# Optimization experiments

Measured on AMD Instinct MI355X. Metric: run time of the kernel, lower is better.

## Reference

```python
import jax, jax.numpy as jnp
import numpy as np

EMBED_DIM = 128
N_EMBED = 10000
INPUT_SHAPE = (8, 64, 32, EMBED_DIM)


def setup_inputs() -> dict:
    key = jax.random.key(0)
    k1, k2 = jax.random.split(key)
    inputs = jax.random.normal(k1, INPUT_SHAPE, dtype=jnp.float32)
    cluster_mean = jax.random.normal(k2, (EMBED_DIM, N_EMBED), dtype=jnp.float32)
    return {"inputs": inputs, "cluster_mean": cluster_mean}


def reference(inputs, cluster_mean):
    embed_dim = cluster_mean.shape[0]
    # Flatten all leading dims: (N, D)
    samples = inputs.reshape(-1, embed_dim)
    # Squared euclidean distance to each code: (N, n_embed)
    dist = (
        jnp.sum(samples ** 2, axis=1, keepdims=True)
        - 2.0 * samples @ cluster_mean
        + jnp.sum(cluster_mean ** 2, axis=0, keepdims=True)
    )
    cluster_index = jnp.argmin(dist, axis=1).reshape(inputs.shape[:-1])
    # Embedding lookup from transposed codebook: (..., D)
    quantize = cluster_mean.T[cluster_index]
    q_loss = jnp.mean((quantize - jax.lax.stop_gradient(inputs)) ** 2)
    e_loss = jnp.mean((jax.lax.stop_gradient(quantize) - inputs) ** 2)
    loss = q_loss + 0.25 * e_loss
    # Straight-through estimator
    outputs = inputs + jax.lax.stop_gradient(quantize - inputs)
    return outputs, loss
```

## Files before the change

kernel.cpp:

```cpp
#include <hip/hip_runtime.h>

#define EMBED 128
#define NCODE 10000
#define NSAMP 16384
#define NCODE_PAD 10240
#define NSPLIT 8
#define SPLIT_CODES 1280
#define NCHUNK 20
#define CHUNK_ELEMS 8192
#define OUT_ELEMS (NSAMP * EMBED)
#define TAU 0.002f
#define NSEG 16

typedef float f32x16 __attribute__((ext_vector_type(16)));
typedef short s16x8 __attribute__((ext_vector_type(8)));
typedef unsigned short ushort_t;
typedef unsigned long long u64;

#define OFF_AH  0
#define OFF_AL  2621440
#define OFF_CT  5242880
#define OFF_CN  10485760
#define OFF_KEY 10526720
#define OFF_C2  11575296
#define OFF_IDX 12099584
#define OFF_RL  12165120
#define OFF_CNT 12230656
#define OFF_BEST 12230720

__device__ __forceinline__ unsigned short f2bf(float f) {
    unsigned u = __float_as_uint(f);
    return (unsigned short)((u + 0x7fffu + ((u >> 16) & 1u)) >> 16);
}
__device__ __forceinline__ float bf2f(unsigned short h) {
    return __uint_as_float(((unsigned)h) << 16);
}
__device__ __forceinline__ unsigned ordf(float f) {
    unsigned u = __float_as_uint(f);
    return (u & 0x80000000u) ? ~u : (u | 0x80000000u);
}
__device__ __forceinline__ float unordf(unsigned o) {
    return __uint_as_float((o & 0x80000000u) ? (o ^ 0x80000000u) : ~o);
}

__global__ __launch_bounds__(256) void prep_norm(const float* __restrict__ C,
                                                 float* __restrict__ cnorm,
                                                 float* __restrict__ out,
                                                 int* __restrict__ counter) {
    int j = blockIdx.x * 256 + threadIdx.x;
    if (j == 0) { out[OUT_ELEMS] = 0.f; *counter = 0; }
    if (j >= NCODE_PAD) return;
    if (j >= NCODE) { cnorm[j] = 3.0e38f; return; }
    float s = 0.f;
#pragma unroll 8
    for (int d = 0; d < EMBED; ++d) {
        float v = C[d * NCODE + j];
        s = fmaf(v, v, s);
    }
    cnorm[j] = s;
}

__global__ __launch_bounds__(256) void prep_c4(const float* __restrict__ C,
                                               ushort_t* __restrict__ Ah,
                                               ushort_t* __restrict__ Al,
                                               float* __restrict__ CT) {
    int o = blockIdx.x * 256 + threadIdx.x;
    int n  = o % NCODE_PAD;
    int kg = o / NCODE_PAD;
    int split = n / SPLIT_CODES;
    int rem   = n % SPLIT_CODES;
    int chunk = rem >> 6;
    int mb    = (rem >> 5) & 1;
    int row   = rem & 31;
    int ks = kg >> 1, kh = kg & 1;
    size_t eoff = (size_t)(split * NCHUNK + chunk) * CHUNK_ELEMS
                + (size_t)(mb * 4096 + (ks * 2 + kh) * 256 + row * 8);
    int k0 = kg * 8;
    float f[8];
#pragma unroll
    for (int j = 0; j < 8; ++j)
        f[j] = (n < NCODE) ? C[(size_t)(k0 + j) * NCODE + n] : 0.f;
    *(float4*)(CT + (size_t)n * EMBED + k0)     = make_float4(f[0], f[1], f[2], f[3]);
    *(float4*)(CT + (size_t)n * EMBED + k0 + 4) = make_float4(f[4], f[5], f[6], f[7]);
    s16x8 vh, vl;
#pragma unroll
    for (int j = 0; j < 8; ++j) {
        unsigned short h = f2bf(f[j]);
        vh[j] = (short)h;
        vl[j] = (short)f2bf(f[j] - bf2f(h));
    }
    *(s16x8*)(Ah + eoff) = vh;
    *(s16x8*)(Al + eoff) = vl;
}

__global__ __launch_bounds__(256, 2) void vq7(const float* __restrict__ X,
                                              const ushort_t* __restrict__ Ah,
                                              const ushort_t* __restrict__ Al,
                                              const float* __restrict__ cnorm,
                                              u64* __restrict__ candKey,
                                              unsigned* __restrict__ cand2) {
    __shared__ ushort_t Bs[2 * 2 * CHUNK_ELEMS];
    __shared__ float cns[SPLIT_CODES];
    const int t    = threadIdx.x;
    const int lane = t & 63;
    const int wave = t >> 6;
    const int ln   = lane & 31;
    const int kh   = lane >> 5;
    const int split = blockIdx.y;
    const int m0    = blockIdx.x * 256;
    const int sbase = split * SPLIT_CODES;

    s16x8 bh[2][8], bl[2][8];
#pragma unroll
    for (int g = 0; g < 2; ++g) {
        int m = m0 + wave * 64 + g * 32 + ln;
#pragma unroll
        for (int ks = 0; ks < 8; ++ks) {
            const float* src = X + (size_t)m * EMBED + ks * 16 + kh * 8;
            float4 f0 = *(const float4*)src;
            float4 f1 = *(const float4*)(src + 4);
            float f[8] = {f0.x, f0.y, f0.z, f0.w, f1.x, f1.y, f1.z, f1.w};
            s16x8 vh, vl;
#pragma unroll
            for (int j = 0; j < 8; ++j) {
                float v = -2.f * f[j];
                unsigned short h = f2bf(v);
                vh[j] = (short)h;
                vl[j] = (short)f2bf(v - bf2f(h));
            }
            bh[g][ks] = vh;
            bl[g][ks] = vl;
        }
    }

    for (int i = t; i < SPLIT_CODES; i += 256) cns[i] = cnorm[sbase + i];

    float v1[2] = {3.4e38f, 3.4e38f}, v2[2] = {3.4e38f, 3.4e38f};
    int   j1[2] = {0, 0};

    auto ldsw = (__attribute__((address_space(3))) ushort_t*)Bs;
    const int woff = wave * 2048;
    const size_t chbase = (size_t)(split * NCHUNK) * CHUNK_ELEMS;

    auto stage = [&](int cc, int buf) {
        const size_t sb = chbase + (size_t)cc * CHUNK_ELEMS;
        const ushort_t* sh = Ah + sb + woff + lane * 8;
        const ushort_t* sl = Al + sb + woff + lane * 8;
        const int db = buf * 2 * CHUNK_ELEMS + woff;
#pragma unroll
        for (int i = 0; i < 4; ++i) {
            __builtin_amdgcn_global_load_lds(
                (const __attribute__((address_space(1))) void*)(sh + i * 512),
                (__attribute__((address_space(3))) void*)(ldsw + db + i * 512),
                16, 0, 0);
            __builtin_amdgcn_global_load_lds(
                (const __attribute__((address_space(1))) void*)(sl + i * 512),
                (__attribute__((address_space(3))) void*)(ldsw + db + CHUNK_ELEMS + i * 512),
                16, 0, 0);
        }
    };

#define MFMA_PHASE(BB, MB, P0, P1)                                            \
    {                                                                         \
        P0 = (f32x16){0,0,0,0,0,0,0,0,0,0,0,0,0,0,0,0};                       \
        P1 = (f32x16){0,0,0,0,0,0,0,0,0,0,0,0,0,0,0,0};                       \
        _Pragma("unroll")                                                     \
        for (int ks = 0; ks < 8; ++ks) {                                      \
            const int fo = (BB) + (MB) * 4096 + (ks * 2 + kh) * 256 + ln * 8; \
            s16x8 a_h = *(const s16x8*)&Bs[fo];                               \
            s16x8 a_l = *(const s16x8*)&Bs[CHUNK_ELEMS + fo];                 \
            P0 = __builtin_amdgcn_mfma_f32_32x32x16_bf16(a_h, bh[0][ks], P0, 0, 0, 0); \
            P1 = __builtin_amdgcn_mfma_f32_32x32x16_bf16(a_h, bh[1][ks], P1, 0, 0, 0); \
            P0 = __builtin_amdgcn_mfma_f32_32x32x16_bf16(a_h, bl[0][ks], P0, 0, 0, 0); \
            P1 = __builtin_amdgcn_mfma_f32_32x32x16_bf16(a_h, bl[1][ks], P1, 0, 0, 0); \
            P0 = __builtin_amdgcn_mfma_f32_32x32x16_bf16(a_l, bh[0][ks], P0, 0, 0, 0); \
            P1 = __builtin_amdgcn_mfma_f32_32x32x16_bf16(a_l, bh[1][ks], P1, 0, 0, 0); \
        }                                                                     \
    }

#define EPI(P0, P1, CB)                                                       \
    {                                                                         \
        _Pragma("unroll")                                                     \
        for (int r = 0; r < 16; ++r) {                                        \
            const int cc = (CB) + ((r & 3) + 8 * (r >> 2));                   \
            const float cn = cns[cc];                                         \
            const int code = sbase + cc;                                      \
            float d0 = P0[r] + cn;                                            \
            v2[0] = fminf(v2[0], fmaxf(d0, v1[0]));                           \
            if (d0 < v1[0]) j1[0] = code;                                     \
            v1[0] = fminf(v1[0], d0);                                         \
            float d1 = P1[r] + cn;                                            \
            v2[1] = fminf(v2[1], fmaxf(d1, v1[1]));                           \
            if (d1 < v1[1]) j1[1] = code;                                     \
            v1[1] = fminf(v1[1], d1);                                         \
        }                                                                     \
    }

    f32x16 aA0, aA1, aB0, aB1;
    int cbA, cbB;

    stage(0, 0);
    __syncthreads();
    {
        stage(1, 1);
        const int cb = 4 * kh;
        MFMA_PHASE(0, 0, aA0, aA1);
        cbA = cb;
        MFMA_PHASE(0, 1, aB0, aB1);
        EPI(aA0, aA1, cbA);
        cbB = cb + 32;
        __syncthreads();
    }

    for (int c = 1; c < NCHUNK; ++c) {
        const int b = c & 1;
        if (c + 1 < NCHUNK) stage(c + 1, 1 - b);
        const int bb = b * 2 * CHUNK_ELEMS;
        const int cb = c * 64 + 4 * kh;

        MFMA_PHASE(bb, 0, aA0, aA1);
        EPI(aB0, aB1, cbB);
        cbA = cb;
        MFMA_PHASE(bb, 1, aB0, aB1);
        EPI(aA0, aA1, cbA);
        cbB = cb + 32;
        __syncthreads();
    }
    EPI(aB0, aB1, cbB);

#pragma unroll
    for (int g = 0; g < 2; ++g) {
        float ov1 = __shfl_xor(v1[g], 32, 64);
        int   oj1 = __shfl_xor(j1[g], 32, 64);
        float ov2 = __shfl_xor(v2[g], 32, 64);
        float hi = fmaxf(v1[g], ov1);
        v2[g] = fminf(fminf(v2[g], ov2), hi);
        if (ov1 < v1[g] || (ov1 == v1[g] && oj1 < j1[g])) { v1[g] = ov1; j1[g] = oj1; }
        if (kh == 0) {
            int m = m0 + wave * 64 + g * 32 + ln;
            candKey[(size_t)m * NSPLIT + split] =
                ((u64)ordf(v1[g]) << 32) | (unsigned)j1[g];
            cand2[(size_t)m * NSPLIT + split] = ordf(v2[g]);
        }
    }
#undef MFMA_PHASE
#undef EPI
}

__global__ __launch_bounds__(256) void outfin_k(const float* __restrict__ X,
                                                const float* __restrict__ CT,
                                                const u64* __restrict__ candKey,
                                                const unsigned* __restrict__ cand2,
                                                int* __restrict__ idxf,
                                                int* __restrict__ rlist,
                                                int* __restrict__ counter,
                                                u64* __restrict__ wsBest,
                                                float* __restrict__ out) {
    __shared__ float red[4];
    const int t = threadIdx.x;
    const int m = blockIdx.x * 8 + (t >> 5);
    const int l = t & 31;

    int code = 0;
    if (l == 0) {
        u64 best = 0xffffffffffffffffull;
        float v2 = 3.4e38f;
#pragma unroll
        for (int s = 0; s < NSPLIT; ++s) {
            u64 k = candKey[(size_t)m * NSPLIT + s];
            unsigned o2 = cand2[(size_t)m * NSPLIT + s];
            if (k < best) {
                if (best != 0xffffffffffffffffull)
                    v2 = fminf(v2, unordf((unsigned)(best >> 32)));
                best = k;
                v2 = fminf(v2, unordf(o2));
            } else {
                v2 = fminf(v2, unordf((unsigned)(k >> 32)));
            }
        }
        code = (int)(unsigned)(best & 0xffffffffu);
        idxf[m] = code;
        float v1 = unordf((unsigned)(best >> 32));
        if (v2 - v1 <= TAU) {
            rlist[atomicAdd(counter, 1)] = m;
            wsBest[m] = 0xffffffffffffffffull;
        }
    }
    code = __shfl(code, 0, 32);

    float4 q = *(const float4*)(CT + (size_t)code * EMBED + l * 4);
    float4 x = *(const float4*)(X + (size_t)m * EMBED + l * 4);
    *(float4*)(out + (size_t)m * EMBED + l * 4) = q;
    float dx = q.x - x.x, dy = q.y - x.y, dz = q.z - x.z, dw = q.w - x.w;
    float lsum = dx * dx + dy * dy + dz * dz + dw * dw;
#pragma unroll
    for (int off = 1; off < 64; off <<= 1) lsum += __shfl_xor(lsum, off, 64);
    if ((t & 63) == 0) red[t >> 6] = lsum;
    __syncthreads();
    if (t == 0)
        atomicAdd(out + OUT_ELEMS,
                  (red[0] + red[1] + red[2] + red[3]) * (1.25f / (float)OUT_ELEMS));
}

__global__ __launch_bounds__(256) void rescue_seg(const float* __restrict__ X,
                                                  const float* __restrict__ CT,
                                                  const float* __restrict__ cnorm,
                                                  const int* __restrict__ rlist,
                                                  const int* __restrict__ counter,
                                                  u64* __restrict__ wsBest) {
    __shared__ float xs[EMBED];
    __shared__ u64 wk[4];
    const int t = threadIdx.x;
    const int lane = t & 63;
    const int wave = t >> 6;
    const int hw = t & 31;
    const int slot = t >> 5;
    const int cnt = *counter;
    const int nw = cnt * NSEG;

    for (int w = blockIdx.x; w < nw; w += gridDim.x) {
        const int s = w >> 4, seg = w & 15;
        const int m = rlist[s];
        __syncthreads();
        if (t < 32) {
            float4 v = *(const float4*)(X + (size_t)m * EMBED + t * 4);
            xs[t * 4 + 0] = v.x; xs[t * 4 + 1] = v.y;
            xs[t * 4 + 2] = v.z; xs[t * 4 + 3] = v.w;
        }
        __syncthreads();
        const float x0 = xs[hw * 4 + 0], x1 = xs[hw * 4 + 1];
        const float x2 = xs[hw * 4 + 2], x3 = xs[hw * 4 + 3];
        const int base = seg * 625;
        const int jend = base + 625;
        u64 bk = 0xffffffffffffffffull;
        for (int it = 0; it < 20; ++it) {
            const int r0 = base + it * 32 + slot * 4;
            float4 c0, c1, c2, c3;
            bool ok0 = (r0 + 0 < jend), ok1 = (r0 + 1 < jend);
            bool ok2 = (r0 + 2 < jend), ok3 = (r0 + 3 < jend);
            c0 = ok0 ? *(const float4*)(CT + (size_t)(r0 + 0) * EMBED + hw * 4) : make_float4(0, 0, 0, 0);
            c1 = ok1 ? *(const float4*)(CT + (size_t)(r0 + 1) * EMBED + hw * 4) : make_float4(0, 0, 0, 0);
            c2 = ok2 ? *(const float4*)(CT + (size_t)(r0 + 2) * EMBED + hw * 4) : make_float4(0, 0, 0, 0);
            c3 = ok3 ? *(const float4*)(CT + (size_t)(r0 + 3) * EMBED + hw * 4) : make_float4(0, 0, 0, 0);
            float p0 = x0 * c0.x, p1 = x0 * c1.x, p2 = x0 * c2.x, p3 = x0 * c3.x;
            p0 = fmaf(x1, c0.y, p0); p1 = fmaf(x1, c1.y, p1);
            p2 = fmaf(x1, c2.y, p2); p3 = fmaf(x1, c3.y, p3);
            p0 = fmaf(x2, c0.z, p0); p1 = fmaf(x2, c1.z, p1);
            p2 = fmaf(x2, c2.z, p2); p3 = fmaf(x2, c3.z, p3);
            p0 = fmaf(x3, c0.w, p0); p1 = fmaf(x3, c1.w, p1);
            p2 = fmaf(x3, c2.w, p2); p3 = fmaf(x3, c3.w, p3);
#pragma unroll
            for (int off = 1; off < 32; off <<= 1) {
                p0 += __shfl_xor(p0, off, 32);
                p1 += __shfl_xor(p1, off, 32);
                p2 += __shfl_xor(p2, off, 32);
                p3 += __shfl_xor(p3, off, 32);
            }
            if (hw == 0) {
                if (ok0) { u64 k = ((u64)ordf(fmaf(-2.f, p0, cnorm[r0 + 0])) << 32) | (unsigned)(r0 + 0); if (k < bk) bk = k; }
                if (ok1) { u64 k = ((u64)ordf(fmaf(-2.f, p1, cnorm[r0 + 1])) << 32) | (unsigned)(r0 + 1); if (k < bk) bk = k; }
                if (ok2) { u64 k = ((u64)ordf(fmaf(-2.f, p2, cnorm[r0 + 2])) << 32) | (unsigned)(r0 + 2); if (k < bk) bk = k; }
                if (ok3) { u64 k = ((u64)ordf(fmaf(-2.f, p3, cnorm[r0 + 3])) << 32) | (unsigned)(r0 + 3); if (k < bk) bk = k; }
            }
        }
#pragma unroll
        for (int off = 1; off < 64; off <<= 1) {
            u64 o = __shfl_xor(bk, off, 64);
            if (o < bk) bk = o;
        }
        if (lane == 0) wk[wave] = bk;
        __syncthreads();
        if (t == 0) {
            u64 b = wk[0];
            if (wk[1] < b) b = wk[1];
            if (wk[2] < b) b = wk[2];
            if (wk[3] < b) b = wk[3];
            atomicMin(&wsBest[m], b);
        }
    }
}

__global__ __launch_bounds__(256) void patch_k(const float* __restrict__ X,
                                               const float* __restrict__ CT,
                                               const int* __restrict__ rlist,
                                               const int* __restrict__ counter,
                                               const u64* __restrict__ wsBest,
                                               const int* __restrict__ idxf,
                                               float* __restrict__ out) {
    const int t = threadIdx.x;
    const int l = t & 31, sl = t >> 5;
    const int cnt = *counter;
    for (int s = blockIdx.x * 8 + sl; s < cnt; s += gridDim.x * 8) {
        int m = rlist[s];
        u64 key = wsBest[m];
        int jn = (int)(unsigned)(key & 0xffffffffu);
        int jo = idxf[m];
        if (jn == jo) continue;
        float4 qn = *(const float4*)(CT + (size_t)jn * EMBED + l * 4);
        float4 qo = *(const float4*)(CT + (size_t)jo * EMBED + l * 4);
        float4 x  = *(const float4*)(X + (size_t)m * EMBED + l * 4);
        *(float4*)(out + (size_t)m * EMBED + l * 4) = qn;
        float dn = (qn.x - x.x) * (qn.x - x.x) + (qn.y - x.y) * (qn.y - x.y)
                 + (qn.z - x.z) * (qn.z - x.z) + (qn.w - x.w) * (qn.w - x.w);
        float dp = (qo.x - x.x) * (qo.x - x.x) + (qo.y - x.y) * (qo.y - x.y)
                 + (qo.z - x.z) * (qo.z - x.z) + (qo.w - x.w) * (qo.w - x.w);
        float delta = dn - dp;
#pragma unroll
        for (int off = 1; off < 32; off <<= 1) delta += __shfl_xor(delta, off, 32);
        if (l == 0)
            atomicAdd(out + OUT_ELEMS, delta * (1.25f / (float)OUT_ELEMS));
    }
}

extern "C" void kernel_launch(void* const* d_in, const int* in_sizes, int n_in,
                              void* d_out, int out_size, void* d_ws, size_t ws_size,
                              hipStream_t stream) {
    const float* X = (const float*)d_in[0];
    const float* C = (const float*)d_in[1];
    float* out = (float*)d_out;
    char* ws = (char*)d_ws;

    ushort_t* Ah = (ushort_t*)(ws + OFF_AH);
    ushort_t* Al = (ushort_t*)(ws + OFF_AL);
    float* CT    = (float*)(ws + OFF_CT);
    float* cnorm = (float*)(ws + OFF_CN);
    u64* candKey = (u64*)(ws + OFF_KEY);
    unsigned* cand2 = (unsigned*)(ws + OFF_C2);
    int* idxf    = (int*)(ws + OFF_IDX);
    int* rlist   = (int*)(ws + OFF_RL);
    int* counter = (int*)(ws + OFF_CNT);
    u64* wsBest  = (u64*)(ws + OFF_BEST);

    prep_norm<<<NCODE_PAD / 256, 256, 0, stream>>>(C, cnorm, out, counter);
    prep_c4<<<(NCODE_PAD * 16) / 256, 256, 0, stream>>>(C, Ah, Al, CT);
    vq7<<<dim3(NSAMP / 256, NSPLIT), 256, 0, stream>>>(X, Ah, Al, cnorm, candKey, cand2);
    outfin_k<<<NSAMP / 8, 256, 0, stream>>>(X, CT, candKey, cand2, idxf, rlist, counter, wsBest, out);
    rescue_seg<<<1024, 256, 0, stream>>>(X, CT, cnorm, rlist, counter, wsBest);
    patch_k<<<64, 256, 0, stream>>>(X, CT, rlist, counter, wsBest, idxf, out);
}
```

Baseline: 253.0 us.

## Load codebook fragments directly from global instead of double-buffered LDS staging

The main distance kernel stops staging codebook hi/lo bf16 chunks into shared memory with async global-to-LDS loads and double buffering. Each wave now reads its MFMA operands straight from global memory, relying on L2/cache reuse. This removes the per-chunk barriers and frees LDS. The grid is also flattened to 1D with the split as the fast index, so blocks sharing a codebook split are spread out. The risk is higher global load latency exposed in the MFMA loop, since nothing prefetches the operands any more.

```diff
diff --git a/kernel.cpp b/kernel.cpp
--- a/kernel.cpp
+++ b/kernel.cpp
@@ -99,15 +99,14 @@
                                               const float* __restrict__ cnorm,
                                               u64* __restrict__ candKey,
                                               unsigned* __restrict__ cand2) {
-    __shared__ ushort_t Bs[2 * 2 * CHUNK_ELEMS];
     __shared__ float cns[SPLIT_CODES];
     const int t    = threadIdx.x;
     const int lane = t & 63;
     const int wave = t >> 6;
     const int ln   = lane & 31;
     const int kh   = lane >> 5;
-    const int split = blockIdx.y;
-    const int m0    = blockIdx.x * 256;
+    const int split = blockIdx.x & 7;
+    const int m0    = (blockIdx.x >> 3) * 256;
     const int sbase = split * SPLIT_CODES;
 
     s16x8 bh[2][8], bl[2][8];
@@ -134,41 +133,22 @@
     }
 
     for (int i = t; i < SPLIT_CODES; i += 256) cns[i] = cnorm[sbase + i];
+    __syncthreads();
 
     float v1[2] = {3.4e38f, 3.4e38f}, v2[2] = {3.4e38f, 3.4e38f};
     int   j1[2] = {0, 0};
 
-    auto ldsw = (__attribute__((address_space(3))) ushort_t*)Bs;
-    const int woff = wave * 2048;
     const size_t chbase = (size_t)(split * NCHUNK) * CHUNK_ELEMS;
 
-    auto stage = [&](int cc, int buf) {
-        const size_t sb = chbase + (size_t)cc * CHUNK_ELEMS;
-        const ushort_t* sh = Ah + sb + woff + lane * 8;
-        const ushort_t* sl = Al + sb + woff + lane * 8;
-        const int db = buf * 2 * CHUNK_ELEMS + woff;
-#pragma unroll
-        for (int i = 0; i < 4; ++i) {
-            __builtin_amdgcn_global_load_lds(
-                (const __attribute__((address_space(1))) void*)(sh + i * 512),
-                (__attribute__((address_space(3))) void*)(ldsw + db + i * 512),
-                16, 0, 0);
-            __builtin_amdgcn_global_load_lds(
-                (const __attribute__((address_space(1))) void*)(sl + i * 512),
-                (__attribute__((address_space(3))) void*)(ldsw + db + CHUNK_ELEMS + i * 512),
-                16, 0, 0);
-        }
-    };
-
-#define MFMA_PHASE(BB, MB, P0, P1)                                            \
+#define MFMA_PHASE(CBE, MB, P0, P1)                                           \
     {                                                                         \
         P0 = (f32x16){0,0,0,0,0,0,0,0,0,0,0,0,0,0,0,0};                       \
         P1 = (f32x16){0,0,0,0,0,0,0,0,0,0,0,0,0,0,0,0};                       \
         _Pragma("unroll")                                                     \
         for (int ks = 0; ks < 8; ++ks) {                                      \
-            const int fo = (BB) + (MB) * 4096 + (ks * 2 + kh) * 256 + ln * 8; \
-            s16x8 a_h = *(const s16x8*)&Bs[fo];                               \
-            s16x8 a_l = *(const s16x8*)&Bs[CHUNK_ELEMS + fo];                 \
+            const size_t fo = (CBE) + (size_t)((MB) * 4096 + (ks * 2 + kh) * 256 + ln * 8); \
+            s16x8 a_h = *(const s16x8*)(Ah + fo);                             \
+            s16x8 a_l = *(const s16x8*)(Al + fo);                             \
             P0 = __builtin_amdgcn_mfma_f32_32x32x16_bf16(a_h, bh[0][ks], P0, 0, 0, 0); \
             P1 = __builtin_amdgcn_mfma_f32_32x32x16_bf16(a_h, bh[1][ks], P1, 0, 0, 0); \
             P0 = __builtin_amdgcn_mfma_f32_32x32x16_bf16(a_h, bl[0][ks], P0, 0, 0, 0); \
@@ -199,32 +179,25 @@
     f32x16 aA0, aA1, aB0, aB1;
     int cbA, cbB;
 
-    stage(0, 0);
-    __syncthreads();
     {
-        stage(1, 1);
         const int cb = 4 * kh;
-        MFMA_PHASE(0, 0, aA0, aA1);
+        MFMA_PHASE(chbase, 0, aA0, aA1);
         cbA = cb;
-        MFMA_PHASE(0, 1, aB0, aB1);
+        MFMA_PHASE(chbase, 1, aB0, aB1);
         EPI(aA0, aA1, cbA);
         cbB = cb + 32;
-        __syncthreads();
     }
 
     for (int c = 1; c < NCHUNK; ++c) {
-        const int b = c & 1;
-        if (c + 1 < NCHUNK) stage(c + 1, 1 - b);
-        const int bb = b * 2 * CHUNK_ELEMS;
+        const size_t cbe = chbase + (size_t)c * CHUNK_ELEMS;
         const int cb = c * 64 + 4 * kh;
 
-        MFMA_PHASE(bb, 0, aA0, aA1);
+        MFMA_PHASE(cbe, 0, aA0, aA1);
         EPI(aB0, aB1, cbB);
         cbA = cb;
-        MFMA_PHASE(bb, 1, aB0, aB1);
+        MFMA_PHASE(cbe, 1, aB0, aB1);
         EPI(aA0, aA1, cbA);
         cbB = cb + 32;
-        __syncthreads();
     }
     EPI(aB0, aB1, cbB);
 
@@ -433,7 +406,7 @@
 
     prep_norm<<<NCODE_PAD / 256, 256, 0, stream>>>(C, cnorm, out, counter);
     prep_c4<<<(NCODE_PAD * 16) / 256, 256, 0, stream>>>(C, Ah, Al, CT);
-    vq7<<<dim3(NSAMP / 256, NSPLIT), 256, 0, stream>>>(X, Ah, Al, cnorm, candKey, cand2);
+    vq7<<<NSAMP / 256 * NSPLIT, 256, 0, stream>>>(X, Ah, Al, cnorm, candKey, cand2);
     outfin_k<<<NSAMP / 8, 256, 0, stream>>>(X, CT, candKey, cand2, idxf, rlist, counter, wsBest, out);
     rescue_seg<<<1024, 256, 0, stream>>>(X, CT, cnorm, rlist, counter, wsBest);
     patch_k<<<64, 256, 0, stream>>>(X, CT, rlist, counter, wsBest, idxf, out);
```

Measured after the change: 406.5 us. +60.7%, slower.

## Fuse codebook prep kernels and seed MFMA accumulators with code norms

Applied to the files above, without the earlier changes.

Merges the norm and layout-conversion prep kernels into one launch that computes per-code squared norms with a shared-memory reduction while writing the bf16 split and transposed codebook. In the main distance kernel, accumulators are initialized from the code norms loaded as float4 vectors, which removes the per-element norm add and scalar LDS load from the epilogue. The split base is added to the code index only once at the end. This saves one kernel launch and epilogue ALU work. In exchange, the prep blocks gain extra barriers, and the column access pattern in prep changes.

```diff
diff --git a/kernel.cpp b/kernel.cpp
--- a/kernel.cpp
+++ b/kernel.cpp
@@ -43,43 +43,36 @@
     return __uint_as_float((o & 0x80000000u) ? (o ^ 0x80000000u) : ~o);
 }
 
-__global__ __launch_bounds__(256) void prep_norm(const float* __restrict__ C,
-                                                 float* __restrict__ cnorm,
-                                                 float* __restrict__ out,
-                                                 int* __restrict__ counter) {
-    int j = blockIdx.x * 256 + threadIdx.x;
-    if (j == 0) { out[OUT_ELEMS] = 0.f; *counter = 0; }
-    if (j >= NCODE_PAD) return;
-    if (j >= NCODE) { cnorm[j] = 3.0e38f; return; }
+__global__ __launch_bounds__(256) void prep_all(const float* __restrict__ C,
+                                                ushort_t* __restrict__ Ah,
+                                                ushort_t* __restrict__ Al,
+                                                float* __restrict__ CT,
+                                                float* __restrict__ cnorm,
+                                                float* __restrict__ out,
+                                                int* __restrict__ counter) {
+    __shared__ float red[256];
+    const int t  = threadIdx.x;
+    const int nl = t & 15;
+    const int kg = t >> 4;
+    const int n  = blockIdx.x * 16 + nl;
+    if (blockIdx.x == 0 && t == 0) { out[OUT_ELEMS] = 0.f; *counter = 0; }
+
+    const int split = n / SPLIT_CODES;
+    const int rem   = n % SPLIT_CODES;
+    const int chunk = rem >> 6;
+    const int mb    = (rem >> 5) & 1;
+    const int row   = rem & 31;
+    const int ks = kg >> 1, kh = kg & 1;
+    const size_t eoff = (size_t)(split * NCHUNK + chunk) * CHUNK_ELEMS
+                      + (size_t)(mb * 4096 + (ks * 2 + kh) * 256 + row * 8);
+    const int k0 = kg * 8;
+    float f[8];
     float s = 0.f;
-#pragma unroll 8
-    for (int d = 0; d < EMBED; ++d) {
-        float v = C[d * NCODE + j];
-        s = fmaf(v, v, s);
-    }
-    cnorm[j] = s;
-}
-
-__global__ __launch_bounds__(256) void prep_c4(const float* __restrict__ C,
-                                               ushort_t* __restrict__ Ah,
-                                               ushort_t* __restrict__ Al,
-                                               float* __restrict__ CT) {
-    int o = blockIdx.x * 256 + threadIdx.x;
-    int n  = o % NCODE_PAD;
-    int kg = o / NCODE_PAD;
-    int split = n / SPLIT_CODES;
-    int rem   = n % SPLIT_CODES;
-    int chunk = rem >> 6;
-    int mb    = (rem >> 5) & 1;
-    int row   = rem & 31;
-    int ks = kg >> 1, kh = kg & 1;
-    size_t eoff = (size_t)(split * NCHUNK + chunk) * CHUNK_ELEMS
-                + (size_t)(mb * 4096 + (ks * 2 + kh) * 256 + row * 8);
-    int k0 = kg * 8;
-    float f[8];
-#pragma unroll
-    for (int j = 0; j < 8; ++j)
+#pragma unroll
+    for (int j = 0; j < 8; ++j) {
         f[j] = (n < NCODE) ? C[(size_t)(k0 + j) * NCODE + n] : 0.f;
+        s = fmaf(f[j], f[j], s);
+    }
     *(float4*)(CT + (size_t)n * EMBED + k0)     = make_float4(f[0], f[1], f[2], f[3]);
     *(float4*)(CT + (size_t)n * EMBED + k0 + 4) = make_float4(f[4], f[5], f[6], f[7]);
     s16x8 vh, vl;
@@ -91,6 +84,19 @@
     }
     *(s16x8*)(Ah + eoff) = vh;
     *(s16x8*)(Al + eoff) = vl;
+
+    red[t] = s;
+    __syncthreads();
+    if (t < 128) red[t] += red[t + 128];
+    __syncthreads();
+    if (t < 64) red[t] += red[t + 64];
+    __syncthreads();
+    if (t < 32) red[t] += red[t + 32];
+    __syncthreads();
+    if (t < 16) {
+        const int nn = blockIdx.x * 16 + t;
+        cnorm[nn] = (nn < NCODE) ? (red[t] + red[t + 16]) : 3.0e38f;
+    }
 }
 
 __global__ __launch_bounds__(256, 2) void vq7(const float* __restrict__ X,
@@ -100,7 +106,7 @@
                                               u64* __restrict__ candKey,
                                               unsigned* __restrict__ cand2) {
     __shared__ ushort_t Bs[2 * 2 * CHUNK_ELEMS];
-    __shared__ float cns[SPLIT_CODES];
+    __shared__ __align__(16) float cns[SPLIT_CODES];
     const int t    = threadIdx.x;
     const int lane = t & 63;
     const int wave = t >> 6;
@@ -160,10 +166,15 @@
         }
     };
 
-#define MFMA_PHASE(BB, MB, P0, P1)                                            \
+#define MFMA_PHASE(BB, MB, CB2, P0, P1)                                       \
     {                                                                         \
-        P0 = (f32x16){0,0,0,0,0,0,0,0,0,0,0,0,0,0,0,0};                       \
-        P1 = (f32x16){0,0,0,0,0,0,0,0,0,0,0,0,0,0,0,0};                       \
+        const float4 q0 = *(const float4*)&cns[(CB2)];                        \
+        const float4 q1 = *(const float4*)&cns[(CB2) + 8];                    \
+        const float4 q2 = *(const float4*)&cns[(CB2) + 16];                   \
+        const float4 q3 = *(const float4*)&cns[(CB2) + 24];                   \
+        P0 = (f32x16){q0.x, q0.y, q0.z, q0.w, q1.x, q1.y, q1.z, q1.w,         \
+                      q2.x, q2.y, q2.z, q2.w, q3.x, q3.y, q3.z, q3.w};        \
+        P1 = P0;                                                              \
         _Pragma("unroll")                                                     \
         for (int ks = 0; ks < 8; ++ks) {                                      \
             const int fo = (BB) + (MB) * 4096 + (ks * 2 + kh) * 256 + ln * 8; \
@@ -178,20 +189,18 @@
         }                                                                     \
     }
 
-#define EPI(P0, P1, CB)                                                       \
+#define EPI(P0, P1, CB2)                                                      \
     {                                                                         \
         _Pragma("unroll")                                                     \
         for (int r = 0; r < 16; ++r) {                                        \
-            const int cc = (CB) + ((r & 3) + 8 * (r >> 2));                   \
-            const float cn = cns[cc];                                         \
-            const int code = sbase + cc;                                      \
-            float d0 = P0[r] + cn;                                            \
+            const int cc = (CB2) + ((r & 3) + 8 * (r >> 2));                  \
+            const float d0 = P0[r];                                           \
+            if (d0 < v1[0]) j1[0] = cc;                                       \
             v2[0] = fminf(v2[0], fmaxf(d0, v1[0]));                           \
-            if (d0 < v1[0]) j1[0] = code;                                     \
             v1[0] = fminf(v1[0], d0);                                         \
-            float d1 = P1[r] + cn;                                            \
+            const float d1 = P1[r];                                           \
+            if (d1 < v1[1]) j1[1] = cc;                                       \
             v2[1] = fminf(v2[1], fmaxf(d1, v1[1]));                           \
-            if (d1 < v1[1]) j1[1] = code;                                     \
             v1[1] = fminf(v1[1], d1);                                         \
         }                                                                     \
     }
@@ -204,9 +213,9 @@
     {
         stage(1, 1);
         const int cb = 4 * kh;
-        MFMA_PHASE(0, 0, aA0, aA1);
+        MFMA_PHASE(0, 0, cb, aA0, aA1);
         cbA = cb;
-        MFMA_PHASE(0, 1, aB0, aB1);
+        MFMA_PHASE(0, 1, cb + 32, aB0, aB1);
         EPI(aA0, aA1, cbA);
         cbB = cb + 32;
         __syncthreads();
@@ -218,10 +227,10 @@
         const int bb = b * 2 * CHUNK_ELEMS;
         const int cb = c * 64 + 4 * kh;
 
-        MFMA_PHASE(bb, 0, aA0, aA1);
+        MFMA_PHASE(bb, 0, cb, aA0, aA1);
         EPI(aB0, aB1, cbB);
         cbA = cb;
-        MFMA_PHASE(bb, 1, aB0, aB1);
+        MFMA_PHASE(bb, 1, cb + 32, aB0, aB1);
         EPI(aA0, aA1, cbA);
         cbB = cb + 32;
         __syncthreads();
@@ -239,7 +248,7 @@
         if (kh == 0) {
             int m = m0 + wave * 64 + g * 32 + ln;
             candKey[(size_t)m * NSPLIT + split] =
-                ((u64)ordf(v1[g]) << 32) | (unsigned)j1[g];
+                ((u64)ordf(v1[g]) << 32) | (unsigned)(sbase + j1[g]);
             cand2[(size_t)m * NSPLIT + split] = ordf(v2[g]);
         }
     }
@@ -431,8 +440,7 @@
     int* counter = (int*)(ws + OFF_CNT);
     u64* wsBest  = (u64*)(ws + OFF_BEST);
 
-    prep_norm<<<NCODE_PAD / 256, 256, 0, stream>>>(C, cnorm, out, counter);
-    prep_c4<<<(NCODE_PAD * 16) / 256, 256, 0, stream>>>(C, Ah, Al, CT);
+    prep_all<<<NCODE_PAD / 16, 256, 0, stream>>>(C, Ah, Al, CT, cnorm, out, counter);
     vq7<<<dim3(NSAMP / 256, NSPLIT), 256, 0, stream>>>(X, Ah, Al, cnorm, candKey, cand2);
     outfin_k<<<NSAMP / 8, 256, 0, stream>>>(X, CT, candKey, cand2, idxf, rlist, counter, wsBest, out);
     rescue_seg<<<1024, 256, 0, stream>>>(X, CT, cnorm, rlist, counter, wsBest);
```

After: 266.2 us. 1.05x slower.
